# Optimization experiments

Hardware: AMD Instinct MI355X
Metric: run time of the kernel (lower is better)

The kernel has to match this reference:

```python
import jax, jax.numpy as jnp
import numpy as np

WS = 8          # window_size
DIM = 384
HEADS = 12
HEAD_DIM = DIM // HEADS
HIDDEN = int(DIM * 2.0)
EPS = 1e-5


def _rel_pos_index(ws):
    # static (N,N) int index into the (2*ws-1)^2 bias table
    coords = np.stack(np.meshgrid(np.arange(ws), np.arange(ws), indexing='ij'))  # (2,ws,ws)
    flat = coords.reshape(2, -1)                      # (2, N)
    rel = flat[:, :, None] - flat[:, None, :]         # (2, N, N)
    rel = rel.transpose(1, 2, 0)                      # (N, N, 2)
    rel[:, :, 0] += ws - 1
    rel[:, :, 1] += ws - 1
    rel[:, :, 0] *= 2 * ws - 1
    return rel.sum(-1)                                # (N, N)

REL_IDX = jnp.asarray(_rel_pos_index(WS))


def _layernorm(x, w, b):
    m = jnp.mean(x, axis=-1, keepdims=True)
    v = jnp.var(x, axis=-1, keepdims=True)
    return (x - m) * jax.lax.rsqrt(v + EPS) * w + b


def setup_inputs() -> dict:
    key = jax.random.key(0)
    ks = jax.random.split(key, 12)
    B, C, H, Wd = 8, DIM, 128, 128
    s = 0.02
    return {
        'x': jax.random.normal(ks[0], (B, C, H, Wd), jnp.float32),
        'H': H,
        'W': Wd,
        'norm1_w': jnp.ones((C,), jnp.float32),
        'norm1_b': jnp.zeros((C,), jnp.float32),
        'qkv_w': jax.random.normal(ks[1], (C, 3 * C), jnp.float32) * s,  # (in,out)
        'qkv_b': jnp.zeros((3 * C,), jnp.float32),
        'proj_w': jax.random.normal(ks[2], (C, C), jnp.float32) * s,
        'proj_b': jnp.zeros((C,), jnp.float32),
        'rel_bias_table': jax.random.normal(ks[3], ((2 * WS - 1) ** 2, HEADS), jnp.float32) * s,
        'norm2_w': jnp.ones((C,), jnp.float32),
        'norm2_b': jnp.zeros((C,), jnp.float32),
        'fc1_w': jax.random.normal(ks[4], (C, HIDDEN), jnp.float32) * s,
        'fc1_b': jnp.zeros((HIDDEN,), jnp.float32),
        'fc2_w': jax.random.normal(ks[5], (HIDDEN, C), jnp.float32) * s,
        'fc2_b': jnp.zeros((C,), jnp.float32),
    }


def reference(x, H, W, norm1_w, norm1_b, qkv_w, qkv_b, proj_w, proj_b,
              rel_bias_table, norm2_w, norm2_b, fc1_w, fc1_b, fc2_w, fc2_b):
    B, C, Hc, Wc = x.shape
    N = WS * WS
    shortcut = x
    # faithful partition: permute to (B,H,W,C) then flat-reshape into 64-token chunks
    xw = jnp.transpose(x, (0, 2, 3, 1)).reshape(B * H * W // N, N, C)
    xn = _layernorm(xw, norm1_w, norm1_b)

    # window attention
    qkv = (xn @ qkv_w + qkv_b).reshape(-1, N, 3, HEADS, HEAD_DIM)
    q, k, v = jnp.moveaxis(qkv, 2, 0)                 # each (B_, N, h, hd)
    q = q * (HEAD_DIM ** -0.5)
    attn = jnp.einsum('bnhd,bmhd->bhnm', q, k)        # (B_, h, N, N)
    bias = rel_bias_table[REL_IDX]                    # (N, N, h)
    attn = attn + jnp.transpose(bias, (2, 0, 1))[None]
    attn = jax.nn.softmax(attn, axis=-1)
    out = jnp.einsum('bhnm,bmhd->bnhd', attn, v).reshape(-1, N, C)
    out = out @ proj_w + proj_b

    # norm2 + MLP (no inner residual; matches source)
    y = _layernorm(out, norm2_w, norm2_b)
    y = jax.nn.gelu(y @ fc1_w + fc1_b, approximate=False) @ fc2_w + fc2_b

    # faithful merge: standard 2D window-merge permute
    y = y.reshape(B, H // WS, W // WS, WS, WS, C)
    y = jnp.transpose(y, (0, 5, 1, 3, 2, 4)).reshape(B, C, H, W)
    return y + shortcut
```

## Files before the change

kernel.cpp:

```cpp
#include <hip/hip_runtime.h>
#include <math.h>

#define HWPIX 16384

typedef unsigned short u16;
typedef __attribute__((ext_vector_type(8))) short short8;
typedef __attribute__((ext_vector_type(4))) float f32x4;

__device__ __forceinline__ float bf2f(u16 h) { return __uint_as_float(((unsigned)h) << 16); }
__device__ __forceinline__ u16 f2bf(float f) {
  unsigned u = __float_as_uint(f);
  u += 0x7fffu + ((u >> 16) & 1u);
  return (u16)(u >> 16);
}

#define MFMA16(a, b, c) __builtin_amdgcn_mfma_f32_16x16x32_bf16((a), (b), (c), 0, 0, 0)

__global__ __launch_bounds__(256) void k0_prep(
    const float* __restrict__ qkv_w, const float* __restrict__ proj_w,
    const float* __restrict__ fc1_w, const float* __restrict__ fc2_w,
    const float* __restrict__ relb,
    u16* __restrict__ wqkv, u16* __restrict__ wproj,
    u16* __restrict__ wfc1, u16* __restrict__ wfc2, float* __restrict__ bias12) {
  int e = blockIdx.x * 256 + threadIdx.x;
  if (e < 442368) { int o = e / 384, i = e % 384; wqkv[e] = f2bf(qkv_w[i * 1152 + o]); return; }
  e -= 442368;
  if (e < 147456) { int o = e / 384, i = e % 384; wproj[e] = f2bf(proj_w[i * 384 + o]); return; }
  e -= 147456;
  if (e < 294912) { int o = e / 384, i = e % 384; wfc1[e] = f2bf(fc1_w[i * 768 + o]); return; }
  e -= 294912;
  if (e < 294912) { int o = e / 768, i = e % 768; wfc2[e] = f2bf(fc2_w[i * 384 + o]); return; }
  e -= 294912;
  if (e < 49152) {
    int h = e / 4096, r = e % 4096, n = r / 64, m = r % 64;
    int dy = n / 8 - m / 8 + 7, dx = n % 8 - m % 8 + 7;
    bias12[e] = relb[(dy * 15 + dx) * 12 + h];
  }
}

__global__ __launch_bounds__(256) void k1_ln1(const float* __restrict__ x,
                                              const float* __restrict__ nw,
                                              const float* __restrict__ nb,
                                              u16* __restrict__ xn) {
  __shared__ alignas(16) u16 raw[64][392];
  __shared__ float psum[4][64], psq[4][64];
  int win = blockIdx.x;
  int b = win >> 8, s = win & 255;
  int wave = threadIdx.x >> 6, lane = threadIdx.x & 63;
  const float* xb = x + (size_t)b * 384 * HWPIX + s * 64 + lane;
  float sum = 0.f, sq = 0.f;
  for (int c = wave; c < 384; c += 4) {
    float v = xb[(size_t)c * HWPIX];
    sum += v; sq += v * v;
    raw[lane][c] = f2bf(v);
  }
  psum[wave][lane] = sum; psq[wave][lane] = sq;
  __syncthreads();
#pragma unroll
  for (int tt = 0; tt < 2; tt++) {
    int t = tt * 32 + wave * 8 + (lane >> 3);
    float s4 = psum[0][t] + psum[1][t] + psum[2][t] + psum[3][t];
    float q4 = psq[0][t] + psq[1][t] + psq[2][t] + psq[3][t];
    float m = s4 * (1.0f / 384.0f);
    float rstd = rsqrtf(q4 * (1.0f / 384.0f) - m * m + 1e-5f);
    u16* orow = xn + ((size_t)win * 64 + t) * 384;
#pragma unroll
    for (int it = 0; it < 12; it++) {
      int c = (lane & 7) * 4 + it * 32;
      ushort4 rv = *(const ushort4*)&raw[t][c];
      float4 nwv = *(const float4*)&nw[c];
      float4 nbv = *(const float4*)&nb[c];
      ushort4 ov;
      ov.x = f2bf((bf2f(rv.x) - m) * rstd * nwv.x + nbv.x);
      ov.y = f2bf((bf2f(rv.y) - m) * rstd * nwv.y + nbv.y);
      ov.z = f2bf((bf2f(rv.z) - m) * rstd * nwv.z + nbv.z);
      ov.w = f2bf((bf2f(rv.w) - m) * rstd * nwv.w + nbv.w);
      *(ushort4*)&orow[c] = ov;
    }
  }
}

__device__ __forceinline__ void tile_step_128(const u16* As, const u16* Bs, int wr, int wc,
                                              int l15, int quad, f32x4 acc[4][4]) {
  short8 af[4], bf[4];
#pragma unroll
  for (int i = 0; i < 4; i++)
    af[i] = *(const short8*)&As[(wr * 64 + i * 16 + l15) * 32 + quad * 8];
#pragma unroll
  for (int j = 0; j < 4; j++)
    bf[j] = *(const short8*)&Bs[(wc * 64 + j * 16 + l15) * 32 + quad * 8];
#pragma unroll
  for (int i = 0; i < 4; i++)
#pragma unroll
    for (int j = 0; j < 4; j++)
      acc[i][j] = MFMA16(af[i], bf[j], acc[i][j]);
}

__global__ __launch_bounds__(256) void k2_qkv(const u16* __restrict__ xn, const u16* __restrict__ wt,
                                              const float* __restrict__ bias,
                                              u16* __restrict__ qb, u16* __restrict__ kb,
                                              u16* __restrict__ vtb) {
  __shared__ alignas(16) u16 As[128 * 32];
  __shared__ alignas(16) u16 Bs[128 * 32];
  int tid = threadIdx.x, lane = tid & 63, wave = tid >> 6;
  int l15 = lane & 15, quad = lane >> 4;
  int wr = wave >> 1, wc = wave & 1;
  int mblk = blockIdx.x % 1024, nblk = blockIdx.x / 1024;
  int row0 = mblk * 128, col0 = nblk * 128;
  f32x4 z = {0.f, 0.f, 0.f, 0.f};
  f32x4 acc[4][4];
#pragma unroll
  for (int i = 0; i < 4; i++)
#pragma unroll
    for (int j = 0; j < 4; j++) acc[i][j] = z;
  int sr = tid >> 2, sc = (tid & 3) * 8;
  for (int k0 = 0; k0 < 384; k0 += 32) {
    __syncthreads();
    *(short8*)&As[sr * 32 + sc] = *(const short8*)&xn[(size_t)(row0 + sr) * 384 + k0 + sc];
    *(short8*)&As[(sr + 64) * 32 + sc] = *(const short8*)&xn[(size_t)(row0 + sr + 64) * 384 + k0 + sc];
    *(short8*)&Bs[sr * 32 + sc] = *(const short8*)&wt[(size_t)(col0 + sr) * 384 + k0 + sc];
    *(short8*)&Bs[(sr + 64) * 32 + sc] = *(const short8*)&wt[(size_t)(col0 + sr + 64) * 384 + k0 + sc];
    __syncthreads();
    tile_step_128(As, Bs, wr, wc, l15, quad, acc);
  }
#pragma unroll
  for (int j = 0; j < 4; j++) {
    int ocol = col0 + wc * 64 + j * 16 + l15;
    float bo = bias[ocol];
    int part = ocol / 384, within = ocol % 384;
    int h = within / 32, d = within % 32;
#pragma unroll
    for (int i = 0; i < 4; i++) {
#pragma unroll
      for (int r = 0; r < 4; r++) {
        int row = row0 + wr * 64 + i * 16 + quad * 4 + r;
        int win = row >> 6, tok = row & 63;
        float val = acc[i][j][r] + bo;
        if (part == 0)
          qb[(size_t)((win * 12 + h) * 64 + tok) * 32 + d] = f2bf(val * 0.17677669529663687f);
        else if (part == 1)
          kb[(size_t)((win * 12 + h) * 64 + tok) * 32 + d] = f2bf(val);
        else
          vtb[(size_t)((win * 12 + h) * 32 + d) * 64 + tok] = f2bf(val);
      }
    }
  }
}

__global__ __launch_bounds__(256) void k3_attn(const u16* __restrict__ qb, const u16* __restrict__ kb,
                                               const u16* __restrict__ vtb,
                                               const float* __restrict__ bias12,
                                               u16* __restrict__ ao) {
  __shared__ alignas(16) u16 P[4][64 * 72];
  int tid = threadIdx.x, lane = tid & 63, wave = tid >> 6;
  int l15 = lane & 15, quad = lane >> 4;
  int wh = blockIdx.x * 4 + wave;
  int win = wh / 12, h = wh % 12;
  const u16* qh = qb + (size_t)wh * 2048;
  const u16* kh = kb + (size_t)wh * 2048;
  const u16* vh = vtb + (size_t)wh * 2048;
  short8 aq[4], bk[4];
#pragma unroll
  for (int t = 0; t < 4; t++) {
    aq[t] = *(const short8*)&qh[(t * 16 + l15) * 32 + quad * 8];
    bk[t] = *(const short8*)&kh[(t * 16 + l15) * 32 + quad * 8];
  }
  f32x4 z = {0.f, 0.f, 0.f, 0.f};
  f32x4 S[4][4];
#pragma unroll
  for (int mt = 0; mt < 4; mt++)
#pragma unroll
    for (int nt = 0; nt < 4; nt++) S[mt][nt] = MFMA16(aq[mt], bk[nt], z);
  const float* bh = bias12 + h * 4096;
#pragma unroll
  for (int mt = 0; mt < 4; mt++)
#pragma unroll
    for (int rr = 0; rr < 4; rr++) {
      int rown = mt * 16 + quad * 4 + rr;
#pragma unroll
      for (int nt = 0; nt < 4; nt++) S[mt][nt][rr] += bh[rown * 64 + nt * 16 + l15];
    }
#pragma unroll
  for (int mt = 0; mt < 4; mt++)
#pragma unroll
    for (int rr = 0; rr < 4; rr++) {
      float mx = S[mt][0][rr];
      mx = fmaxf(mx, S[mt][1][rr]);
      mx = fmaxf(mx, S[mt][2][rr]);
      mx = fmaxf(mx, S[mt][3][rr]);
#pragma unroll
      for (int m = 1; m < 16; m <<= 1) mx = fmaxf(mx, __shfl_xor(mx, m, 64));
      float pv[4], se = 0.f;
#pragma unroll
      for (int nt = 0; nt < 4; nt++) { pv[nt] = __expf(S[mt][nt][rr] - mx); se += pv[nt]; }
#pragma unroll
      for (int m = 1; m < 16; m <<= 1) se += __shfl_xor(se, m, 64);
      float inv = 1.0f / se;
      int rown = mt * 16 + quad * 4 + rr;
#pragma unroll
      for (int nt = 0; nt < 4; nt++)
        P[wave][rown * 72 + nt * 16 + l15] = f2bf(pv[nt] * inv);
    }
  __syncthreads();
  short8 ap[4][2], bv[2][2];
#pragma unroll
  for (int mt = 0; mt < 4; mt++)
#pragma unroll
    for (int ks = 0; ks < 2; ks++)
      ap[mt][ks] = *(const short8*)&P[wave][(mt * 16 + l15) * 72 + ks * 32 + quad * 8];
#pragma unroll
  for (int nt = 0; nt < 2; nt++)
#pragma unroll
    for (int ks = 0; ks < 2; ks++)
      bv[nt][ks] = *(const short8*)&vh[(nt * 16 + l15) * 64 + ks * 32 + quad * 8];
  f32x4 O[4][2];
#pragma unroll
  for (int mt = 0; mt < 4; mt++)
#pragma unroll
    for (int nt = 0; nt < 2; nt++) {
      O[mt][nt] = z;
      O[mt][nt] = MFMA16(ap[mt][0], bv[nt][0], O[mt][nt]);
      O[mt][nt] = MFMA16(ap[mt][1], bv[nt][1], O[mt][nt]);
    }
#pragma unroll
  for (int mt = 0; mt < 4; mt++)
#pragma unroll
    for (int nt = 0; nt < 2; nt++)
#pragma unroll
      for (int r = 0; r < 4; r++) {
        int tok = mt * 16 + quad * 4 + r, d = nt * 16 + l15;
        ao[((size_t)win * 64 + tok) * 384 + h * 32 + d] = f2bf(O[mt][nt][r]);
      }
}

__global__ __launch_bounds__(256) void k4_proj_ln2(const u16* __restrict__ ao, const u16* __restrict__ wt,
                                                   const float* __restrict__ pb,
                                                   const float* __restrict__ nw,
                                                   const float* __restrict__ nb,
                                                   u16* __restrict__ y1) {
  __shared__ alignas(16) u16 As[64 * 32];
  __shared__ alignas(16) u16 Bs[384 * 32];
  __shared__ float redS[4][64], redQ[4][64];
  int tid = threadIdx.x, lane = tid & 63, wave = tid >> 6;
  int l15 = lane & 15, quad = lane >> 4;
  size_t row0 = (size_t)blockIdx.x * 64;
  f32x4 z = {0.f, 0.f, 0.f, 0.f};
  f32x4 acc[4][6];
#pragma unroll
  for (int i = 0; i < 4; i++)
#pragma unroll
    for (int j = 0; j < 6; j++) acc[i][j] = z;
  int sr = tid >> 2, sc = (tid & 3) * 8;
  for (int k0 = 0; k0 < 384; k0 += 32) {
    __syncthreads();
    *(short8*)&As[sr * 32 + sc] = *(const short8*)&ao[(row0 + sr) * 384 + k0 + sc];
#pragma unroll
    for (int i = 0; i < 6; i++) {
      int e = tid * 8 + i * 2048;
      int r = e >> 5;
      *(short8*)&Bs[e] = *(const short8*)&wt[(size_t)r * 384 + k0 + (e & 31)];
    }
    __syncthreads();
    short8 af[4];
#pragma unroll
    for (int i = 0; i < 4; i++) af[i] = *(const short8*)&As[(i * 16 + l15) * 32 + quad * 8];
#pragma unroll
    for (int j = 0; j < 6; j++) {
      short8 bf = *(const short8*)&Bs[(wave * 96 + j * 16 + l15) * 32 + quad * 8];
#pragma unroll
      for (int i = 0; i < 4; i++) acc[i][j] = MFMA16(af[i], bf, acc[i][j]);
    }
  }
  float pb6[6], nw6[6], nb6[6];
#pragma unroll
  for (int j = 0; j < 6; j++) {
    int col = wave * 96 + j * 16 + l15;
    pb6[j] = pb[col]; nw6[j] = nw[col]; nb6[j] = nb[col];
  }
#pragma unroll
  for (int i = 0; i < 4; i++)
#pragma unroll
    for (int r = 0; r < 4; r++) {
      float s = 0.f, q = 0.f;
#pragma unroll
      for (int j = 0; j < 6; j++) {
        float v = acc[i][j][r] + pb6[j];
        s += v; q += v * v;
      }
#pragma unroll
      for (int m = 1; m < 16; m <<= 1) { s += __shfl_xor(s, m, 64); q += __shfl_xor(q, m, 64); }
      if (l15 == 0) {
        redS[wave][i * 16 + quad * 4 + r] = s;
        redQ[wave][i * 16 + quad * 4 + r] = q;
      }
    }
  __syncthreads();
#pragma unroll
  for (int i = 0; i < 4; i++)
#pragma unroll
    for (int r = 0; r < 4; r++) {
      int row = i * 16 + quad * 4 + r;
      float s = redS[0][row] + redS[1][row] + redS[2][row] + redS[3][row];
      float q = redQ[0][row] + redQ[1][row] + redQ[2][row] + redQ[3][row];
      float m = s * (1.0f / 384.0f);
      float rstd = rsqrtf(q * (1.0f / 384.0f) - m * m + 1e-5f);
#pragma unroll
      for (int j = 0; j < 6; j++) {
        int col = wave * 96 + j * 16 + l15;
        float v = acc[i][j][r] + pb6[j];
        y1[(row0 + row) * 384 + col] = f2bf((v - m) * rstd * nw6[j] + nb6[j]);
      }
    }
}

__global__ __launch_bounds__(256) void k5_fc1gelu(const u16* __restrict__ y1, const u16* __restrict__ wt,
                                                  const float* __restrict__ bias,
                                                  u16* __restrict__ hm) {
  __shared__ alignas(16) u16 As[128 * 32];
  __shared__ alignas(16) u16 Bs[128 * 32];
  int tid = threadIdx.x, lane = tid & 63, wave = tid >> 6;
  int l15 = lane & 15, quad = lane >> 4;
  int wr = wave >> 1, wc = wave & 1;
  int mblk = blockIdx.x % 1024, nblk = blockIdx.x / 1024;
  int row0 = mblk * 128, col0 = nblk * 128;
  f32x4 z = {0.f, 0.f, 0.f, 0.f};
  f32x4 acc[4][4];
#pragma unroll
  for (int i = 0; i < 4; i++)
#pragma unroll
    for (int j = 0; j < 4; j++) acc[i][j] = z;
  int sr = tid >> 2, sc = (tid & 3) * 8;
  for (int k0 = 0; k0 < 384; k0 += 32) {
    __syncthreads();
    *(short8*)&As[sr * 32 + sc] = *(const short8*)&y1[(size_t)(row0 + sr) * 384 + k0 + sc];
    *(short8*)&As[(sr + 64) * 32 + sc] = *(const short8*)&y1[(size_t)(row0 + sr + 64) * 384 + k0 + sc];
    *(short8*)&Bs[sr * 32 + sc] = *(const short8*)&wt[(size_t)(col0 + sr) * 384 + k0 + sc];
    *(short8*)&Bs[(sr + 64) * 32 + sc] = *(const short8*)&wt[(size_t)(col0 + sr + 64) * 384 + k0 + sc];
    __syncthreads();
    tile_step_128(As, Bs, wr, wc, l15, quad, acc);
  }
#pragma unroll
  for (int j = 0; j < 4; j++) {
    int ocol = col0 + wc * 64 + j * 16 + l15;
    float bo = bias[ocol];
#pragma unroll
    for (int i = 0; i < 4; i++)
#pragma unroll
      for (int r = 0; r < 4; r++) {
        int row = row0 + wr * 64 + i * 16 + quad * 4 + r;
        float val = acc[i][j][r] + bo;
        float g = 0.5f * val * (1.0f + erff(val * 0.70710678118654752f));
        hm[(size_t)row * 768 + ocol] = f2bf(g);
      }
  }
}

__global__ __launch_bounds__(256) void k6_fc2_merge(const u16* __restrict__ hm, const u16* __restrict__ wt,
                                                    const float* __restrict__ b2,
                                                    const float* __restrict__ x,
                                                    float* __restrict__ out) {
  __shared__ alignas(16) u16 As[128 * 32];
  __shared__ alignas(16) u16 Bs[128 * 32];
  __shared__ alignas(16) u16 TB[128][132];
  int tid = threadIdx.x, lane = tid & 63, wave = tid >> 6;
  int l15 = lane & 15, quad = lane >> 4;
  int wr = wave >> 1, wc = wave & 1;
  int bi = blockIdx.x;
  int ct = bi % 3; bi /= 3;
  int jh = bi % 8; bi /= 8;
  int ih = bi % 16; bi /= 16;
  int b = bi;
  int tbase = (b * 256 + ih * 16) * 64 + jh * 8;
  f32x4 z = {0.f, 0.f, 0.f, 0.f};
  f32x4 acc[4][4];
#pragma unroll
  for (int i = 0; i < 4; i++)
#pragma unroll
    for (int j = 0; j < 4; j++) acc[i][j] = z;
  int sr = tid >> 2, sc = (tid & 3) * 8;
  int sr2 = sr + 64;
  int t0 = tbase + (sr >> 3) * 64 + (sr & 7);
  int t1 = tbase + (sr2 >> 3) * 64 + (sr2 & 7);
  for (int k0 = 0; k0 < 768; k0 += 32) {
    __syncthreads();
    *(short8*)&As[sr * 32 + sc] = *(const short8*)&hm[(size_t)t0 * 768 + k0 + sc];
    *(short8*)&As[sr2 * 32 + sc] = *(const short8*)&hm[(size_t)t1 * 768 + k0 + sc];
    *(short8*)&Bs[sr * 32 + sc] = *(const short8*)&wt[(size_t)(ct * 128 + sr) * 768 + k0 + sc];
    *(short8*)&Bs[sr2 * 32 + sc] = *(const short8*)&wt[(size_t)(ct * 128 + sr2) * 768 + k0 + sc];
    __syncthreads();
    tile_step_128(As, Bs, wr, wc, l15, quad, acc);
  }
#pragma unroll
  for (int jj = 0; jj < 4; jj++) {
    int col = wc * 64 + jj * 16 + l15;
    float bb = b2[ct * 128 + col];
#pragma unroll
    for (int ii = 0; ii < 4; ii++)
#pragma unroll
      for (int r = 0; r < 4; r++) {
        int row = wr * 64 + ii * 16 + quad * 4 + r;
        TB[col][row] = f2bf(acc[ii][jj][r] + bb);
      }
  }
  __syncthreads();
  int hout = ih * 8 + jh;
  int wq = (lane & 31) * 4;
  int chalf = wave * 2 + (lane >> 5);
#pragma unroll
  for (int it = 0; it < 16; it++) {
    int cl = it * 8 + chalf;
    size_t gidx = (((size_t)b * 384 + ct * 128 + cl) * 128 + hout) * 128 + wq;
    float4 xv = *(const float4*)&x[gidx];
    ushort4 tv = *(const ushort4*)&TB[cl][wq];
    float4 ov;
    ov.x = bf2f(tv.x) + xv.x;
    ov.y = bf2f(tv.y) + xv.y;
    ov.z = bf2f(tv.z) + xv.z;
    ov.w = bf2f(tv.w) + xv.w;
    *(float4*)&out[gidx] = ov;
  }
}

extern "C" void kernel_launch(void* const* d_in, const int* in_sizes, int n_in,
                              void* d_out, int out_size, void* d_ws, size_t ws_size,
                              hipStream_t stream) {
  const float* x = (const float*)d_in[0];
  const float* n1w = (const float*)d_in[3];
  const float* n1b = (const float*)d_in[4];
  const float* qkvw = (const float*)d_in[5];
  const float* qkvb = (const float*)d_in[6];
  const float* projw = (const float*)d_in[7];
  const float* projb = (const float*)d_in[8];
  const float* relb = (const float*)d_in[9];
  const float* n2w = (const float*)d_in[10];
  const float* n2b = (const float*)d_in[11];
  const float* fc1w = (const float*)d_in[12];
  const float* fc1b = (const float*)d_in[13];
  const float* fc2w = (const float*)d_in[14];
  const float* fc2b = (const float*)d_in[15];

  char* w = (char*)d_ws;
  u16* wqkv = (u16*)w;  w += 884736;
  u16* wproj = (u16*)w; w += 294912;
  u16* wfc1 = (u16*)w;  w += 589824;
  u16* wfc2 = (u16*)w;  w += 589824;
  float* bias12 = (float*)w; w += 196608;
  u16* bufA = (u16*)w; w += 100663296;
  u16* bufB = (u16*)w; w += 100663296;
  u16* bufC = (u16*)w; w += 100663296;

  u16* xn = bufA;
  u16* qb = (u16*)d_out;
  u16* kb = qb + 50331648;
  u16* vtb = bufB;
  u16* ao = bufC;
  u16* y1 = bufA;
  u16* hm = bufB;
  float* out = (float*)d_out;

  k0_prep<<<dim3(4800), dim3(256), 0, stream>>>(qkvw, projw, fc1w, fc2w, relb,
                                                wqkv, wproj, wfc1, wfc2, bias12);
  k1_ln1<<<dim3(2048), dim3(256), 0, stream>>>(x, n1w, n1b, xn);
  k2_qkv<<<dim3(9216), dim3(256), 0, stream>>>(xn, wqkv, qkvb, qb, kb, vtb);
  k3_attn<<<dim3(6144), dim3(256), 0, stream>>>(qb, kb, vtb, bias12, ao);
  k4_proj_ln2<<<dim3(2048), dim3(256), 0, stream>>>(ao, wproj, projb, n2w, n2b, y1);
  k5_fc1gelu<<<dim3(6144), dim3(256), 0, stream>>>(y1, wfc1, fc1b, hm);
  k6_fc2_merge<<<dim3(3072), dim3(256), 0, stream>>>(hm, wfc2, fc2b, x, out);
}
```

Before: 1.603 ms.

## Use direct global-to-LDS loads and LDS-staged coalesced epilogues in GEMM kernels

Replaces the register-staged global-to-shared tile loads in the qkv, proj, fc1 and fc2 GEMMs with global_load_lds 16-byte direct transfers. The qkv and fc1 epilogues now write results into a shared-memory tile aliased over the operand buffers and then store them to global memory as coalesced 16-byte vectors, instead of scattered 2-byte stores. Block index ordering is changed so that consecutive blocks share the same row tile across column blocks, and fc2 aliases its transpose buffer with the operand tiles to cut LDS use. This adds extra barriers, and the direct-to-LDS path depends on the exact per-wave lane-to-address layout being correct.

Measured after the change: 1.315 ms. 1.22x faster.

```diff
diff --git a/kernel.cpp b/kernel.cpp
--- a/kernel.cpp
+++ b/kernel.cpp
@@ -15,6 +15,12 @@
 }
 
 #define MFMA16(a, b, c) __builtin_amdgcn_mfma_f32_16x16x32_bf16((a), (b), (c), 0, 0, 0)
+
+__device__ __forceinline__ void gl_lds16(const void* g, void* l) {
+  __builtin_amdgcn_global_load_lds(
+      (const __attribute__((address_space(1))) unsigned int*)g,
+      (__attribute__((address_space(3))) unsigned int*)l, 16, 0, 0);
+}
 
 __global__ __launch_bounds__(256) void k0_prep(
     const float* __restrict__ qkv_w, const float* __restrict__ proj_w,
@@ -100,50 +106,87 @@
                                               const float* __restrict__ bias,
                                               u16* __restrict__ qb, u16* __restrict__ kb,
                                               u16* __restrict__ vtb) {
-  __shared__ alignas(16) u16 As[128 * 32];
-  __shared__ alignas(16) u16 Bs[128 * 32];
+  __shared__ alignas(16) u16 smem[17408];
+  u16* As = smem;
+  u16* Bs = smem + 4096;
+  u16* tile = smem;
   int tid = threadIdx.x, lane = tid & 63, wave = tid >> 6;
   int l15 = lane & 15, quad = lane >> 4;
   int wr = wave >> 1, wc = wave & 1;
-  int mblk = blockIdx.x % 1024, nblk = blockIdx.x / 1024;
+  int nblk = blockIdx.x % 9, mblk = blockIdx.x / 9;
   int row0 = mblk * 128, col0 = nblk * 128;
+  int part = nblk / 3, subcol0 = (nblk % 3) * 128;
   f32x4 z = {0.f, 0.f, 0.f, 0.f};
   f32x4 acc[4][4];
 #pragma unroll
   for (int i = 0; i < 4; i++)
 #pragma unroll
     for (int j = 0; j < 4; j++) acc[i][j] = z;
-  int sr = tid >> 2, sc = (tid & 3) * 8;
+  int lrow = lane >> 2, lcol = (lane & 3) * 8;
+  const u16* ga0 = &xn[(size_t)(row0 + wave * 32 + lrow) * 384 + lcol];
+  const u16* ga1 = ga0 + 16 * 384;
+  const u16* gb0 = &wt[(size_t)(col0 + wave * 32 + lrow) * 384 + lcol];
+  const u16* gb1 = gb0 + 16 * 384;
+  u16* lA0 = &As[(wave * 32) * 32];
+  u16* lA1 = &As[(wave * 32 + 16) * 32];
+  u16* lB0 = &Bs[(wave * 32) * 32];
+  u16* lB1 = &Bs[(wave * 32 + 16) * 32];
   for (int k0 = 0; k0 < 384; k0 += 32) {
     __syncthreads();
-    *(short8*)&As[sr * 32 + sc] = *(const short8*)&xn[(size_t)(row0 + sr) * 384 + k0 + sc];
-    *(short8*)&As[(sr + 64) * 32 + sc] = *(const short8*)&xn[(size_t)(row0 + sr + 64) * 384 + k0 + sc];
-    *(short8*)&Bs[sr * 32 + sc] = *(const short8*)&wt[(size_t)(col0 + sr) * 384 + k0 + sc];
-    *(short8*)&Bs[(sr + 64) * 32 + sc] = *(const short8*)&wt[(size_t)(col0 + sr + 64) * 384 + k0 + sc];
+    gl_lds16(ga0 + k0, lA0);
+    gl_lds16(ga1 + k0, lA1);
+    gl_lds16(gb0 + k0, lB0);
+    gl_lds16(gb1 + k0, lB1);
     __syncthreads();
     tile_step_128(As, Bs, wr, wc, l15, quad, acc);
   }
-#pragma unroll
-  for (int j = 0; j < 4; j++) {
-    int ocol = col0 + wc * 64 + j * 16 + l15;
-    float bo = bias[ocol];
-    int part = ocol / 384, within = ocol % 384;
-    int h = within / 32, d = within % 32;
-#pragma unroll
-    for (int i = 0; i < 4; i++) {
-#pragma unroll
-      for (int r = 0; r < 4; r++) {
-        int row = row0 + wr * 64 + i * 16 + quad * 4 + r;
-        int win = row >> 6, tok = row & 63;
-        float val = acc[i][j][r] + bo;
-        if (part == 0)
-          qb[(size_t)((win * 12 + h) * 64 + tok) * 32 + d] = f2bf(val * 0.17677669529663687f);
-        else if (part == 1)
-          kb[(size_t)((win * 12 + h) * 64 + tok) * 32 + d] = f2bf(val);
-        else
-          vtb[(size_t)((win * 12 + h) * 32 + d) * 64 + tok] = f2bf(val);
-      }
-    }
+  __syncthreads();
+  if (part < 2) {
+    float s = (part == 0) ? 0.17677669529663687f : 1.0f;
+#pragma unroll
+    for (int j = 0; j < 4; j++) {
+      int col = wc * 64 + j * 16 + l15;
+      float bo = bias[part * 384 + subcol0 + col];
+#pragma unroll
+      for (int i = 0; i < 4; i++)
+#pragma unroll
+        for (int r = 0; r < 4; r++) {
+          int row = wr * 64 + i * 16 + quad * 4 + r;
+          tile[row * 136 + col] = f2bf((acc[i][j][r] + bo) * s);
+        }
+    }
+  } else {
+#pragma unroll
+    for (int j = 0; j < 4; j++) {
+      int col = wc * 64 + j * 16 + l15;
+      float bo = bias[768 + subcol0 + col];
+#pragma unroll
+      for (int i = 0; i < 4; i++) {
+        int rowst = wr * 64 + i * 16 + quad * 4;
+        ushort4 pk;
+        pk.x = f2bf(acc[i][j][0] + bo);
+        pk.y = f2bf(acc[i][j][1] + bo);
+        pk.z = f2bf(acc[i][j][2] + bo);
+        pk.w = f2bf(acc[i][j][3] + bo);
+        *(ushort4*)&tile[col * 136 + rowst] = pk;
+      }
+    }
+  }
+  __syncthreads();
+  int hb = subcol0 >> 5;
+  int win0 = row0 >> 6;
+  u16* dst0 = (part == 0) ? qb : (part == 1) ? kb : vtb;
+#pragma unroll
+  for (int c = 0; c < 8; c++) {
+    int wl = c >> 2, hl = c & 3;
+    int wh = (win0 + wl) * 12 + hb + hl;
+    u16* dst = dst0 + (size_t)wh * 2048 + tid * 8;
+    short8 v;
+    if (part < 2)
+      v = *(const short8*)&tile[(wl * 64 + (tid >> 2)) * 136 + hl * 32 + (tid & 3) * 8];
+    else
+      v = *(const short8*)&tile[(hl * 32 + (tid >> 3)) * 136 + wl * 64 + (tid & 7) * 8];
+    *(short8*)dst = v;
   }
 }
 
@@ -250,16 +293,21 @@
   for (int i = 0; i < 4; i++)
 #pragma unroll
     for (int j = 0; j < 6; j++) acc[i][j] = z;
-  int sr = tid >> 2, sc = (tid & 3) * 8;
+  int lrow = lane >> 2, lcol = (lane & 3) * 8;
+  const u16* ga = &ao[(row0 + wave * 16 + lrow) * 384 + lcol];
+  u16* lA = &As[(wave * 16) * 32];
+  const u16* gB[6];
+  u16* lB[6];
+#pragma unroll
+  for (int t = 0; t < 6; t++) {
+    gB[t] = &wt[(size_t)(wave * 96 + t * 16 + lrow) * 384 + lcol];
+    lB[t] = &Bs[(wave * 96 + t * 16) * 32];
+  }
   for (int k0 = 0; k0 < 384; k0 += 32) {
     __syncthreads();
-    *(short8*)&As[sr * 32 + sc] = *(const short8*)&ao[(row0 + sr) * 384 + k0 + sc];
-#pragma unroll
-    for (int i = 0; i < 6; i++) {
-      int e = tid * 8 + i * 2048;
-      int r = e >> 5;
-      *(short8*)&Bs[e] = *(const short8*)&wt[(size_t)r * 384 + k0 + (e & 31)];
-    }
+    gl_lds16(ga + k0, lA);
+#pragma unroll
+    for (int t = 0; t < 6; t++) gl_lds16(gB[t] + k0, lB[t]);
     __syncthreads();
     short8 af[4];
 #pragma unroll
@@ -316,12 +364,14 @@
 __global__ __launch_bounds__(256) void k5_fc1gelu(const u16* __restrict__ y1, const u16* __restrict__ wt,
                                                   const float* __restrict__ bias,
                                                   u16* __restrict__ hm) {
-  __shared__ alignas(16) u16 As[128 * 32];
-  __shared__ alignas(16) u16 Bs[128 * 32];
+  __shared__ alignas(16) u16 smem[17408];
+  u16* As = smem;
+  u16* Bs = smem + 4096;
+  u16* tile = smem;
   int tid = threadIdx.x, lane = tid & 63, wave = tid >> 6;
   int l15 = lane & 15, quad = lane >> 4;
   int wr = wave >> 1, wc = wave & 1;
-  int mblk = blockIdx.x % 1024, nblk = blockIdx.x / 1024;
+  int nblk = blockIdx.x % 6, mblk = blockIdx.x / 6;
   int row0 = mblk * 128, col0 = nblk * 128;
   f32x4 z = {0.f, 0.f, 0.f, 0.f};
   f32x4 acc[4][4];
@@ -329,29 +379,45 @@
   for (int i = 0; i < 4; i++)
 #pragma unroll
     for (int j = 0; j < 4; j++) acc[i][j] = z;
-  int sr = tid >> 2, sc = (tid & 3) * 8;
+  int lrow = lane >> 2, lcol = (lane & 3) * 8;
+  const u16* ga0 = &y1[(size_t)(row0 + wave * 32 + lrow) * 384 + lcol];
+  const u16* ga1 = ga0 + 16 * 384;
+  const u16* gb0 = &wt[(size_t)(col0 + wave * 32 + lrow) * 384 + lcol];
+  const u16* gb1 = gb0 + 16 * 384;
+  u16* lA0 = &As[(wave * 32) * 32];
+  u16* lA1 = &As[(wave * 32 + 16) * 32];
+  u16* lB0 = &Bs[(wave * 32) * 32];
+  u16* lB1 = &Bs[(wave * 32 + 16) * 32];
   for (int k0 = 0; k0 < 384; k0 += 32) {
     __syncthreads();
-    *(short8*)&As[sr * 32 + sc] = *(const short8*)&y1[(size_t)(row0 + sr) * 384 + k0 + sc];
-    *(short8*)&As[(sr + 64) * 32 + sc] = *(const short8*)&y1[(size_t)(row0 + sr + 64) * 384 + k0 + sc];
-    *(short8*)&Bs[sr * 32 + sc] = *(const short8*)&wt[(size_t)(col0 + sr) * 384 + k0 + sc];
-    *(short8*)&Bs[(sr + 64) * 32 + sc] = *(const short8*)&wt[(size_t)(col0 + sr + 64) * 384 + k0 + sc];
+    gl_lds16(ga0 + k0, lA0);
+    gl_lds16(ga1 + k0, lA1);
+    gl_lds16(gb0 + k0, lB0);
+    gl_lds16(gb1 + k0, lB1);
     __syncthreads();
     tile_step_128(As, Bs, wr, wc, l15, quad, acc);
   }
+  __syncthreads();
 #pragma unroll
   for (int j = 0; j < 4; j++) {
-    int ocol = col0 + wc * 64 + j * 16 + l15;
-    float bo = bias[ocol];
+    int col = wc * 64 + j * 16 + l15;
+    float bo = bias[col0 + col];
 #pragma unroll
     for (int i = 0; i < 4; i++)
 #pragma unroll
       for (int r = 0; r < 4; r++) {
-        int row = row0 + wr * 64 + i * 16 + quad * 4 + r;
+        int row = wr * 64 + i * 16 + quad * 4 + r;
         float val = acc[i][j][r] + bo;
         float g = 0.5f * val * (1.0f + erff(val * 0.70710678118654752f));
-        hm[(size_t)row * 768 + ocol] = f2bf(g);
-      }
+        tile[row * 136 + col] = f2bf(g);
+      }
+  }
+  __syncthreads();
+#pragma unroll
+  for (int it = 0; it < 8; it++) {
+    int row = it * 16 + (tid >> 4), colp = (tid & 15) * 8;
+    short8 v = *(const short8*)&tile[row * 136 + colp];
+    *(short8*)&hm[(size_t)(row0 + row) * 768 + col0 + colp] = v;
   }
 }
 
@@ -359,9 +425,10 @@
                                                     const float* __restrict__ b2,
                                                     const float* __restrict__ x,
                                                     float* __restrict__ out) {
-  __shared__ alignas(16) u16 As[128 * 32];
-  __shared__ alignas(16) u16 Bs[128 * 32];
-  __shared__ alignas(16) u16 TB[128][132];
+  __shared__ alignas(16) u16 smem[16896];
+  u16* As = smem;
+  u16* Bs = smem + 4096;
+  u16* TB = smem;
   int tid = threadIdx.x, lane = tid & 63, wave = tid >> 6;
   int l15 = lane & 15, quad = lane >> 4;
   int wr = wave >> 1, wc = wave & 1;
@@ -377,19 +444,28 @@
   for (int i = 0; i < 4; i++)
 #pragma unroll
     for (int j = 0; j < 4; j++) acc[i][j] = z;
-  int sr = tid >> 2, sc = (tid & 3) * 8;
-  int sr2 = sr + 64;
-  int t0 = tbase + (sr >> 3) * 64 + (sr & 7);
-  int t1 = tbase + (sr2 >> 3) * 64 + (sr2 & 7);
+  int lrow = lane >> 2, lcol = (lane & 3) * 8;
+  int tr0 = wave * 32 + lrow, tr1 = tr0 + 16;
+  int tok0 = tbase + (tr0 >> 3) * 64 + (tr0 & 7);
+  int tok1 = tbase + (tr1 >> 3) * 64 + (tr1 & 7);
+  const u16* ga0 = &hm[(size_t)tok0 * 768 + lcol];
+  const u16* ga1 = &hm[(size_t)tok1 * 768 + lcol];
+  const u16* gb0 = &wt[(size_t)(ct * 128 + tr0) * 768 + lcol];
+  const u16* gb1 = &wt[(size_t)(ct * 128 + tr1) * 768 + lcol];
+  u16* lA0 = &As[(wave * 32) * 32];
+  u16* lA1 = &As[(wave * 32 + 16) * 32];
+  u16* lB0 = &Bs[(wave * 32) * 32];
+  u16* lB1 = &Bs[(wave * 32 + 16) * 32];
   for (int k0 = 0; k0 < 768; k0 += 32) {
     __syncthreads();
-    *(short8*)&As[sr * 32 + sc] = *(const short8*)&hm[(size_t)t0 * 768 + k0 + sc];
-    *(short8*)&As[sr2 * 32 + sc] = *(const short8*)&hm[(size_t)t1 * 768 + k0 + sc];
-    *(short8*)&Bs[sr * 32 + sc] = *(const short8*)&wt[(size_t)(ct * 128 + sr) * 768 + k0 + sc];
-    *(short8*)&Bs[sr2 * 32 + sc] = *(const short8*)&wt[(size_t)(ct * 128 + sr2) * 768 + k0 + sc];
+    gl_lds16(ga0 + k0, lA0);
+    gl_lds16(ga1 + k0, lA1);
+    gl_lds16(gb0 + k0, lB0);
+    gl_lds16(gb1 + k0, lB1);
     __syncthreads();
     tile_step_128(As, Bs, wr, wc, l15, quad, acc);
   }
+  __syncthreads();
 #pragma unroll
   for (int jj = 0; jj < 4; jj++) {
     int col = wc * 64 + jj * 16 + l15;
@@ -399,7 +475,7 @@
 #pragma unroll
       for (int r = 0; r < 4; r++) {
         int row = wr * 64 + ii * 16 + quad * 4 + r;
-        TB[col][row] = f2bf(acc[ii][jj][r] + bb);
+        TB[col * 132 + row] = f2bf(acc[ii][jj][r] + bb);
       }
   }
   __syncthreads();
@@ -411,7 +487,7 @@
     int cl = it * 8 + chalf;
     size_t gidx = (((size_t)b * 384 + ct * 128 + cl) * 128 + hout) * 128 + wq;
     float4 xv = *(const float4*)&x[gidx];
-    ushort4 tv = *(const ushort4*)&TB[cl][wq];
+    ushort4 tv = *(const ushort4*)&TB[cl * 132 + wq];
     float4 ov;
     ov.x = bf2f(tv.x) + xv.x;
     ov.y = bf2f(tv.y) + xv.y;
```
